# Optimization experiments

Hardware: AMD Instinct MI355X
Metric: run time of the kernel (lower is better)

## Reference

```python
import jax, jax.numpy as jnp
import numpy as np

BS, IN_F, OUT_F = 1024, 128, 100000
M, S, ALPHA = 0.35, 30.0, 0.5


def _l2norm(x):
    # F.normalize: x / max(||x||, eps)
    n = jnp.sqrt(jnp.sum(x * x, axis=-1, keepdims=True))
    return x / jnp.maximum(n, 1e-12)


def setup_inputs() -> dict:
    key = jax.random.key(0)
    k1, k2, k3 = jax.random.split(key, 3)
    return {
        "input": jax.random.normal(k1, (BS, IN_F), dtype=jnp.float32),
        "label": jax.random.randint(k2, (BS,), 0, OUT_F, dtype=jnp.int64),
        "weight": jax.random.normal(k3, (OUT_F, IN_F), dtype=jnp.float32),
    }


def reference(input, label, weight):
    wn = _l2norm(weight)                      # [nc, d]
    fn = _l2norm(input)                       # [bs, d]
    logits = jnp.einsum('bd,cd->bc', fn, wn)  # [bs, nc] cosine sims
    bs = fn.shape[0]
    rows = jnp.arange(bs)

    pos = jnp.take_along_axis(logits, label[:, None], axis=1)[:, 0] * S  # [bs]
    # negatives: all classes except the label (replaces masked_select + view)
    neg = (logits * S).at[rows, label].set(-jnp.inf)
    lse_neg = jax.nn.logsumexp(neg, axis=1)   # [bs]

    # loss = mean(log(1 + exp(m + lse_neg - pos)))
    loss = jnp.mean(jax.nn.softplus(M + lse_neg - pos))

    # weight.data update: per-class mean of normalized features for classes
    # present in the batch (the torch loop is exactly a segment-mean; note
    # weight_update aliases weight.data so the final blend is a no-op and the
    # result is simply: present rows <- class mean, other rows unchanged).
    sums = jax.ops.segment_sum(fn, label, num_segments=OUT_F)                # [nc, d]
    counts = jax.ops.segment_sum(jnp.ones((bs,), fn.dtype), label, num_segments=OUT_F)
    present = counts > 0
    class_mean = sums / jnp.maximum(counts, 1.0)[:, None]
    new_weight = jnp.where(present[:, None], class_mean, weight)

    return loss, new_weight
```

## Files before the change

kernel.cpp:

```cpp
#include <hip/hip_runtime.h>

#define BS 1024
#define D 128
#define NC 100000
#define NCP 100096
#define NTILES 782
#define S_SCALE 30.0f
#define MARGIN 0.35f
#define GRIDX 48
#define GRIDY 16
#define S2LOG2E 43.2808512f

typedef __attribute__((ext_vector_type(8))) short bf16x8;
typedef __attribute__((ext_vector_type(4))) float f32x4;

__device__ __forceinline__ unsigned short f2bf(float f) {
    union { float f; unsigned u; } x; x.f = f;
    unsigned u = x.u;
    u += 0x7FFFu + ((u >> 16) & 1u);
    return (unsigned short)(u >> 16);
}


__global__ void prep_fn(const float* __restrict__ inp, const int* __restrict__ label,
                        const float* __restrict__ wt,
                        float* __restrict__ fn_f32, unsigned short* __restrict__ fn_fr,
                        float* __restrict__ counts, float* __restrict__ pos) {
    int row = blockIdx.x;
    int lane = threadIdx.x;
    float2 v = *(const float2*)(inp + row * D + lane * 2);
    float s = v.x * v.x + v.y * v.y;
    #pragma unroll
    for (int m = 1; m < 64; m <<= 1) s += __shfl_xor(s, m);
    float inv = 1.0f / fmaxf(sqrtf(s), 1e-12f);
    float a = v.x * inv, b = v.y * inv;
    *(float2*)(fn_f32 + row * D + lane * 2) = make_float2(a, b);
    unsigned pack = (unsigned)f2bf(a) | ((unsigned)f2bf(b) << 16);
    ((unsigned*)fn_fr)[(row >> 4) * 1024 + (lane >> 2) * 64 + ((row & 15) << 2) + (lane & 3)] = pack;

    int c = label[row];
    float2 wv = *(const float2*)(wt + c * D + lane * 2);
    float sw_ = wv.x * wv.x + wv.y * wv.y;
    float dt  = wv.x * a + wv.y * b;
    #pragma unroll
    for (int m = 1; m < 64; m <<= 1) { sw_ += __shfl_xor(sw_, m); dt += __shfl_xor(dt, m); }
    if (lane == 0) {
        float invw = 1.0f / fmaxf(sqrtf(sw_), 1e-12f);
        pos[row] = S_SCALE * dt * invw;
        atomicAdd(counts + c, 1.0f);
    }
}

__global__ void prep_wn(const float* __restrict__ wt, const float* __restrict__ counts,
                        unsigned short* __restrict__ wn_fr, float* __restrict__ outw) {
    int wv = threadIdx.x >> 6, lane = threadIdx.x & 63;
    int row = blockIdx.x * 4 + wv;
    unsigned* dst = (unsigned*)wn_fr + (row >> 4) * 1024 + (lane >> 2) * 64 +
                    ((row & 15) << 2) + (lane & 3);
    if (row < NC) {
        float2 v = *(const float2*)(wt + row * D + lane * 2);
        float s = v.x * v.x + v.y * v.y;
        #pragma unroll
        for (int m = 1; m < 64; m <<= 1) s += __shfl_xor(s, m);
        float inv = 1.0f / fmaxf(sqrtf(s), 1e-12f);
        *dst = (unsigned)f2bf(v.x * inv) | ((unsigned)f2bf(v.y * inv) << 16);
        float cnt = counts[row];
        float2 o = (cnt > 0.0f) ? make_float2(0.0f, 0.0f) : v;
        *(float2*)(outw + row * D + lane * 2) = o;
    } else {
        *dst = 0u;
    }
}

__global__ __launch_bounds__(256, 3) void main_gemm(
    const unsigned short* __restrict__ fnfr, const unsigned short* __restrict__ wnfr,
    float* __restrict__ sumexp) {
    __shared__ float red[256];
    int tid = threadIdx.x;
    int lane = tid & 63, w = tid >> 6;
    int quad = lane >> 4, l15 = lane & 15;
    int rowbase = blockIdx.y * 64;

    bf16x8 af[4][4];
    {
        const char* gA = (const char*)fnfr + (rowbase >> 4) * 4096 + lane * 16;
        #pragma unroll
        for (int mt = 0; mt < 4; mt++)
            #pragma unroll
            for (int ks = 0; ks < 4; ks++)
                af[ks][mt] = *(const bf16x8*)(gA + mt * 4096 + ks * 1024);
    }

    float sums[16];
    #pragma unroll
    for (int i = 0; i < 16; i++) sums[i] = 0.0f;

    const char* gB = (const char*)wnfr + (size_t)blockIdx.x * 32768 + w * 8192 + lane * 16;
    const long long step = (long long)GRIDX * 32768;

    bf16x8 b[2][4];
    #pragma unroll
    for (int nt = 0; nt < 2; nt++)
        #pragma unroll
        for (int ks = 0; ks < 4; ks++)
            b[nt][ks] = *(const bf16x8*)(gB + nt * 4096 + ks * 1024);

    for (int tile = blockIdx.x; tile < NTILES; tile += GRIDX) {
        f32x4 acc[4][2];
        #pragma unroll
        for (int mt = 0; mt < 4; mt++)
            #pragma unroll
            for (int nt = 0; nt < 2; nt++)
                acc[mt][nt] = (f32x4){0.0f, 0.0f, 0.0f, 0.0f};

        #pragma unroll
        for (int ks = 0; ks < 4; ks++)
            #pragma unroll
            for (int mt = 0; mt < 4; mt++)
                #pragma unroll
                for (int nt = 0; nt < 2; nt++)
                    acc[mt][nt] = __builtin_amdgcn_mfma_f32_16x16x32_bf16(
                        af[ks][mt], b[nt][ks], acc[mt][nt], 0, 0, 0);

        gB += step;
        if (tile + GRIDX < NTILES) {
            #pragma unroll
            for (int nt = 0; nt < 2; nt++)
                #pragma unroll
                for (int ks = 0; ks < 4; ks++)
                    b[nt][ks] = *(const bf16x8*)(gB + nt * 4096 + ks * 1024);
        }

        #pragma unroll
        for (int mt = 0; mt < 4; mt++)
            #pragma unroll
            for (int nt = 0; nt < 2; nt++)
                #pragma unroll
                for (int r = 0; r < 4; r++)
                    sums[mt * 4 + r] +=
                        __builtin_amdgcn_exp2f(fmaf(acc[mt][nt][r], S2LOG2E, -S2LOG2E));
    }

    #pragma unroll
    for (int mt = 0; mt < 4; mt++) {
        #pragma unroll
        for (int r = 0; r < 4; r++) {
            float s = sums[mt * 4 + r];
            s += __shfl_xor(s, 1);
            s += __shfl_xor(s, 2);
            s += __shfl_xor(s, 4);
            s += __shfl_xor(s, 8);
            if (l15 == 0) red[w * 64 + mt * 16 + quad * 4 + r] = s;
        }
    }
    __syncthreads();
    if (tid < 64) {
        float s = red[tid] + red[64 + tid] + red[128 + tid] + red[192 + tid];
        atomicAdd(sumexp + rowbase + tid, s);
    }
}

__global__ void loss_k(const float* __restrict__ sumexp, const float* __restrict__ pos,
                       float* __restrict__ out) {
    __shared__ float red[256];
    int t = threadIdx.x;
    float acc = 0.0f;
    #pragma unroll
    for (int i = 0; i < 4; i++) {
        int r = t + i * 256;
        float p = pos[r];
        float sneg = fmaxf(sumexp[r] - __expf(p - 30.0f), 1e-38f);
        float lse = 30.0f + logf(sneg);
        float z = MARGIN + lse - p;
        acc += fmaxf(z, 0.0f) + log1pf(__expf(-fabsf(z)));
    }
    red[t] = acc;
    __syncthreads();
    for (int s = 128; s > 0; s >>= 1) {
        if (t < s) red[t] += red[t + s];
        __syncthreads();
    }
    if (t == 0) out[0] = red[0] * (1.0f / 1024.0f);
}

__global__ void addmean_k(const float* __restrict__ fn_f32, const int* __restrict__ label,
                          const float* __restrict__ counts, float* __restrict__ outw) {
    int b = blockIdx.x, t = threadIdx.x;
    int c = label[b];
    float cnt = counts[c];
    atomicAdd(outw + c * D + t, fn_f32[b * D + t] / cnt);
}

extern "C" void kernel_launch(void* const* d_in, const int* in_sizes, int n_in,
                              void* d_out, int out_size, void* d_ws, size_t ws_size,
                              hipStream_t stream) {
    (void)in_sizes; (void)n_in; (void)out_size; (void)ws_size;
    const float* inp   = (const float*)d_in[0];
    const int*   label = (const int*)d_in[1];
    const float* wt    = (const float*)d_in[2];
    float* out = (float*)d_out;

    char* w = (char*)d_ws;
    float*          fn_f32 = (float*)(w);
    unsigned short* fn_fr  = (unsigned short*)(w + 524288);
    unsigned short* wn_fr  = (unsigned short*)(w + 786432);
    float*          sumexp = (float*)(w + 26411008);
    float*          counts = (float*)(w + 26415104);
    float*          pos    = (float*)(w + 26815104);

    hipMemsetAsync(w + 26411008, 0, 404096, stream);

    prep_fn<<<BS, 64, 0, stream>>>(inp, label, wt, fn_f32, fn_fr, counts, pos);
    prep_wn<<<NCP / 4, 256, 0, stream>>>(wt, counts, wn_fr, out + 1);
    main_gemm<<<dim3(GRIDX, GRIDY), 256, 0, stream>>>(fn_fr, wn_fr, sumexp);
    addmean_k<<<BS, D, 0, stream>>>(fn_f32, label, counts, out + 1);
    loss_k<<<1, 256, 0, stream>>>(sumexp, pos, out);
}
```

Before: 157.5 us.

## Keep weight tiles resident and stream batch through GEMM instead

New measurement: 169.3 us. 7.5% more time.

```diff
diff --git a/kernel.cpp b/kernel.cpp
--- a/kernel.cpp
+++ b/kernel.cpp
@@ -7,8 +7,6 @@
 #define NTILES 782
 #define S_SCALE 30.0f
 #define MARGIN 0.35f
-#define GRIDX 48
-#define GRIDY 16
 #define S2LOG2E 43.2808512f
 
 typedef __attribute__((ext_vector_type(8))) short bf16x8;
@@ -26,8 +24,8 @@
                         const float* __restrict__ wt,
                         float* __restrict__ fn_f32, unsigned short* __restrict__ fn_fr,
                         float* __restrict__ counts, float* __restrict__ pos) {
-    int row = blockIdx.x;
-    int lane = threadIdx.x;
+    int row = blockIdx.x * 4 + (threadIdx.x >> 6);
+    int lane = threadIdx.x & 63;
     float2 v = *(const float2*)(inp + row * D + lane * 2);
     float s = v.x * v.x + v.y * v.y;
     #pragma unroll
@@ -75,15 +73,20 @@
 __global__ __launch_bounds__(256, 3) void main_gemm(
     const unsigned short* __restrict__ fnfr, const unsigned short* __restrict__ wnfr,
     float* __restrict__ sumexp) {
-    __shared__ float red[256];
+    __shared__ float red[1024];
     int tid = threadIdx.x;
     int lane = tid & 63, w = tid >> 6;
-    int quad = lane >> 4, l15 = lane & 15;
-    int rowbase = blockIdx.y * 64;
+    int l15 = lane & 15;
+    int cls_half = w >> 1;
+    int bat_half = w & 1;
+
+    #pragma unroll
+    for (int i = 0; i < 4; i++) red[tid + i * 256] = 0.0f;
 
     bf16x8 af[4][4];
     {
-        const char* gA = (const char*)fnfr + (rowbase >> 4) * 4096 + lane * 16;
+        const char* gA = (const char*)wnfr + (size_t)blockIdx.x * 32768 +
+                         cls_half * 16384 + lane * 16;
         #pragma unroll
         for (int mt = 0; mt < 4; mt++)
             #pragma unroll
@@ -91,12 +94,9 @@
                 af[ks][mt] = *(const bf16x8*)(gA + mt * 4096 + ks * 1024);
     }
 
-    float sums[16];
-    #pragma unroll
-    for (int i = 0; i < 16; i++) sums[i] = 0.0f;
-
-    const char* gB = (const char*)wnfr + (size_t)blockIdx.x * 32768 + w * 8192 + lane * 16;
-    const long long step = (long long)GRIDX * 32768;
+    __syncthreads();
+
+    const char* gB = (const char*)fnfr + bat_half * 8192 + lane * 16;
 
     bf16x8 b[2][4];
     #pragma unroll
@@ -105,7 +105,7 @@
         for (int ks = 0; ks < 4; ks++)
             b[nt][ks] = *(const bf16x8*)(gB + nt * 4096 + ks * 1024);
 
-    for (int tile = blockIdx.x; tile < NTILES; tile += GRIDX) {
+    for (int c = 0; c < 16; c++) {
         f32x4 acc[4][2];
         #pragma unroll
         for (int mt = 0; mt < 4; mt++)
@@ -122,41 +122,37 @@
                     acc[mt][nt] = __builtin_amdgcn_mfma_f32_16x16x32_bf16(
                         af[ks][mt], b[nt][ks], acc[mt][nt], 0, 0, 0);
 
-        gB += step;
-        if (tile + GRIDX < NTILES) {
+        if (c < 15) {
+            const char* gBn = gB + (c + 1) * 16384;
             #pragma unroll
             for (int nt = 0; nt < 2; nt++)
                 #pragma unroll
                 for (int ks = 0; ks < 4; ks++)
-                    b[nt][ks] = *(const bf16x8*)(gB + nt * 4096 + ks * 1024);
+                    b[nt][ks] = *(const bf16x8*)(gBn + nt * 4096 + ks * 1024);
         }
 
+        float s0 = 0.0f, s1 = 0.0f;
         #pragma unroll
         for (int mt = 0; mt < 4; mt++)
             #pragma unroll
-            for (int nt = 0; nt < 2; nt++)
-                #pragma unroll
-                for (int r = 0; r < 4; r++)
-                    sums[mt * 4 + r] +=
-                        __builtin_amdgcn_exp2f(fmaf(acc[mt][nt][r], S2LOG2E, -S2LOG2E));
-    }
-
-    #pragma unroll
-    for (int mt = 0; mt < 4; mt++) {
-        #pragma unroll
-        for (int r = 0; r < 4; r++) {
-            float s = sums[mt * 4 + r];
-            s += __shfl_xor(s, 1);
-            s += __shfl_xor(s, 2);
-            s += __shfl_xor(s, 4);
-            s += __shfl_xor(s, 8);
-            if (l15 == 0) red[w * 64 + mt * 16 + quad * 4 + r] = s;
+            for (int r = 0; r < 4; r++) {
+                s0 += __builtin_amdgcn_exp2f(fmaf(acc[mt][0][r], S2LOG2E, -S2LOG2E));
+                s1 += __builtin_amdgcn_exp2f(fmaf(acc[mt][1][r], S2LOG2E, -S2LOG2E));
+            }
+        s0 += __shfl_xor(s0, 16); s0 += __shfl_xor(s0, 32);
+        s1 += __shfl_xor(s1, 16); s1 += __shfl_xor(s1, 32);
+        if (lane < 16) {
+            int base = c * 64 + bat_half * 32 + l15;
+            atomicAdd(&red[base], s0);
+            atomicAdd(&red[base + 16], s1);
         }
     }
+
     __syncthreads();
-    if (tid < 64) {
-        float s = red[tid] + red[64 + tid] + red[128 + tid] + red[192 + tid];
-        atomicAdd(sumexp + rowbase + tid, s);
+    #pragma unroll
+    for (int i = 0; i < 4; i++) {
+        int idx = tid + i * 256;
+        atomicAdd(sumexp + idx, red[idx]);
     }
 }
 
@@ -210,9 +206,9 @@
 
     hipMemsetAsync(w + 26411008, 0, 404096, stream);
 
-    prep_fn<<<BS, 64, 0, stream>>>(inp, label, wt, fn_f32, fn_fr, counts, pos);
+    prep_fn<<<BS / 4, 256, 0, stream>>>(inp, label, wt, fn_f32, fn_fr, counts, pos);
     prep_wn<<<NCP / 4, 256, 0, stream>>>(wt, counts, wn_fr, out + 1);
-    main_gemm<<<dim3(GRIDX, GRIDY), 256, 0, stream>>>(fn_fr, wn_fr, sumexp);
+    main_gemm<<<NTILES, 256, 0, stream>>>(fn_fr, wn_fr, sumexp);
     addmean_k<<<BS, D, 0, stream>>>(fn_f32, label, counts, out + 1);
     loss_k<<<1, 256, 0, stream>>>(sumexp, pos, out);
 }
```
